# Performance work log

Measured on AMD Instinct MI355X. Metric: run time of the kernel, lower is better.

The kernel has to match this reference:

```python
import jax, jax.numpy as jnp
import numpy as np

B, L, D = 8, 2048, 64


def setup_inputs() -> dict:
    key = jax.random.key(0)
    kq, kk, kv = jax.random.split(key, 3)
    query = jax.random.normal(kq, (B, L, D), dtype=jnp.float32)
    key_t = jax.random.normal(kk, (B, L, D), dtype=jnp.float32)
    value = jax.random.normal(kv, (B, L, D), dtype=jnp.float32)
    return {"query": query, "key": key_t, "value": value}


def reference(query, key, value):
    d = query.shape[-1]
    # e = Q K^T / sqrt(d_k)   -> [B, Lq, Lk]
    scale = 1.0 / np.sqrt(float(d)).astype(np.float32)
    e = jnp.einsum("bqd,bkd->bqk", query, key) * scale
    # stable softmax over keys (matches exp(e - max)/sum in source)
    attention = jax.nn.softmax(e, axis=-1)
    # v = A V   -> [B, Lq, Dv]
    return jnp.einsum("bqk,bkd->bqd", attention, value)
```

## Files before the change

### kernel.cpp

```cpp
#include <hip/hip_runtime.h>


#define B_ 8
#define L_ 2048
#define D_ 64
#define NT 256

typedef _Float16 half8_t __attribute__((ext_vector_type(8)));
typedef _Float16 half4_t __attribute__((ext_vector_type(4)));
typedef float f32x4 __attribute__((ext_vector_type(4)));

#define SCALE_LOG2E 0.1803368801111244f

__global__ __launch_bounds__(NT) void prepass_frag(
    const float* __restrict__ K, const float* __restrict__ V,
    _Float16* __restrict__ K16F, _Float16* __restrict__ VT16F)
{
    const int blk = blockIdx.x;
    const int t = threadIdx.x;
    if (blk < 512) {
        const int b  = blk & 7;
        const int kt = blk >> 3;
        const int p    = t >> 6;
        const int lane = t & 63;
        const int quad = lane >> 4;
        const int l15  = lane & 15;
        const int s = p >> 1, c = p & 1;
        const int row = kt * 32 + s * 16 + l15;
        const float* kp = K + ((size_t)b * L_ + row) * D_ + c * 32 + quad * 8;
        const float4 f0 = *(const float4*)kp;
        const float4 f1 = *(const float4*)(kp + 4);
        half8_t w;
        w[0] = (_Float16)f0.x; w[1] = (_Float16)f0.y;
        w[2] = (_Float16)f0.z; w[3] = (_Float16)f0.w;
        w[4] = (_Float16)f1.x; w[5] = (_Float16)f1.y;
        w[6] = (_Float16)f1.z; w[7] = (_Float16)f1.w;
        *(half8_t*)&K16F[((size_t)(b * 64 + kt) * 4 + p) * 512 + lane * 8] = w;
    } else {
        const int vb = blk - 512;
        const int b  = vb & 7;
        const int kt = vb >> 3;
        #pragma unroll
        for (int i = 0; i < 2; ++i) {
            const int slot = i * NT + t;
            const int p    = slot >> 6;
            const int lane = slot & 63;
            const int quad = lane >> 4;
            const int l15  = lane & 15;
            const int d = p >> 1, ks = p & 1;
            const int row = kt * 32 + ks * 16 + quad * 4;
            const int col = d * 16 + l15;
            const float* vp = V + ((size_t)b * L_ + row) * D_ + col;
            half4_t a;
            a[0] = (_Float16)vp[0];
            a[1] = (_Float16)vp[D_];
            a[2] = (_Float16)vp[2 * D_];
            a[3] = (_Float16)vp[3 * D_];
            *(half4_t*)&VT16F[((size_t)(b * 64 + kt) * 4 + d) * 512 + lane * 8 + ks * 4] = a;
        }
    }
}


#define LOADK(KT, BK)                                                           \
    {                                                                           \
        const int ktc_ = (KT) & 63;                                             \
        _Pragma("unroll") for (int s = 0; s < 2; ++s)                           \
        _Pragma("unroll") for (int c = 0; c < 2; ++c)                           \
            BK[s][c] = *(const half8_t*)&KbF[((size_t)ktc_ * 4 + s * 2 + c) * 512 + lane * 8]; \
    }

#define LOADV(KT, AV)                                                           \
    {                                                                           \
        const int ktc_ = (KT) & 63;                                             \
        _Pragma("unroll") for (int d = 0; d < 4; ++d)                           \
            AV[d] = *(const half8_t*)&VbF[((size_t)ktc_ * 4 + d) * 512 + lane * 8]; \
    }

#define PROC(BK, AV)                                                            \
    {                                                                           \
        half4_t pb[2][2];                                                       \
        _Pragma("unroll") for (int ks = 0; ks < 2; ++ks)                        \
        _Pragma("unroll") for (int qs = 0; qs < 2; ++qs) {                      \
            f32x4 acc = (f32x4){0.f, 0.f, 0.f, 0.f};                            \
            acc = __builtin_amdgcn_mfma_f32_16x16x32_f16(BK[ks][0], bq[qs][0], acc, 0, 0, 0); \
            acc = __builtin_amdgcn_mfma_f32_16x16x32_f16(BK[ks][1], bq[qs][1], acc, 0, 0, 0); \
            const float p0 = __builtin_exp2f(acc[0]);                           \
            const float p1 = __builtin_exp2f(acc[1]);                           \
            const float p2 = __builtin_exp2f(acc[2]);                           \
            const float p3 = __builtin_exp2f(acc[3]);                           \
            lacc[qs] += (p0 + p1) + (p2 + p3);                                  \
            half4_t pv;                                                         \
            pv[0] = (_Float16)p0; pv[1] = (_Float16)p1;                         \
            pv[2] = (_Float16)p2; pv[3] = (_Float16)p3;                         \
            pb[ks][qs] = pv;                                                    \
        }                                                                       \
        _Pragma("unroll") for (int d = 0; d < 4; ++d) {                         \
            const half4_t alo = __builtin_shufflevector(AV[d], AV[d], 0, 1, 2, 3); \
            const half4_t ahi = __builtin_shufflevector(AV[d], AV[d], 4, 5, 6, 7); \
            _Pragma("unroll") for (int qs = 0; qs < 2; ++qs) {                  \
                ofr[qs][d] = __builtin_amdgcn_mfma_f32_16x16x16f16(alo, pb[0][qs], ofr[qs][d], 0, 0, 0); \
                ofr[qs][d] = __builtin_amdgcn_mfma_f32_16x16x16f16(ahi, pb[1][qs], ofr[qs][d], 0, 0, 0); \
            }                                                                   \
        }                                                                       \
    }

__global__ __launch_bounds__(1024) void attn_q64w16(
    const float* __restrict__ Q,
    const _Float16* __restrict__ K16F,
    const _Float16* __restrict__ VT16F,
    float* __restrict__ O)
{
    __shared__ float Ored[1024 * 17];
    __shared__ float Lred[512];

    const int t    = threadIdx.x;
    const int wave = t >> 6;
    const int lane = t & 63;
    const int quad = lane >> 4;
    const int l15  = lane & 15;
    const int kg   = wave >> 1;
    const int qg   = wave & 1;

    const int b   = blockIdx.x & 7;
    const int qbi = blockIdx.x >> 3;
    const int qb  = qbi * 64;
    const int q0  = qb + qg * 32;
    const int kt0 = kg * 8;

    const _Float16* KbF = K16F + (size_t)b * 64 * 4 * 512;
    const _Float16* VbF = VT16F + (size_t)b * 64 * 4 * 512;

    half8_t bq[2][2];
    #pragma unroll
    for (int qs = 0; qs < 2; ++qs) {
        const float* qp = Q + ((size_t)b * L_ + q0 + qs * 16 + l15) * D_ + quad * 8;
        #pragma unroll
        for (int c = 0; c < 2; ++c) {
            const float4 f0 = *(const float4*)(qp + c * 32);
            const float4 f1 = *(const float4*)(qp + c * 32 + 4);
            bq[qs][c][0] = (_Float16)(f0.x * SCALE_LOG2E);
            bq[qs][c][1] = (_Float16)(f0.y * SCALE_LOG2E);
            bq[qs][c][2] = (_Float16)(f0.z * SCALE_LOG2E);
            bq[qs][c][3] = (_Float16)(f0.w * SCALE_LOG2E);
            bq[qs][c][4] = (_Float16)(f1.x * SCALE_LOG2E);
            bq[qs][c][5] = (_Float16)(f1.y * SCALE_LOG2E);
            bq[qs][c][6] = (_Float16)(f1.z * SCALE_LOG2E);
            bq[qs][c][7] = (_Float16)(f1.w * SCALE_LOG2E);
        }
    }

    f32x4 ofr[2][4];
    #pragma unroll
    for (int qs = 0; qs < 2; ++qs)
        #pragma unroll
        for (int d = 0; d < 4; ++d)
            ofr[qs][d] = (f32x4){0.f, 0.f, 0.f, 0.f};
    float lacc[2] = {0.f, 0.f};

    half8_t bkA[2][2], bkB[2][2], av[4];
    LOADK(kt0, bkA);
    for (int it = 0; it < 4; ++it) {
        const int kta = kt0 + it * 2;
        LOADK(kta + 1, bkB);
        LOADV(kta, av);
        PROC(bkA, av);
        LOADK(kta + 2, bkA);
        LOADV(kta + 1, av);
        PROC(bkB, av);
    }

    float lsum[2];
    #pragma unroll
    for (int qs = 0; qs < 2; ++qs) {
        float v = lacc[qs];
        v += __shfl_xor(v, 16, 64);
        v += __shfl_xor(v, 32, 64);
        lsum[qs] = v;
    }
    if (quad == 0) {
        Lred[wave * 32 + l15]      = lsum[0];
        Lred[wave * 32 + 16 + l15] = lsum[1];
    }

    #pragma unroll
    for (int qs = 0; qs < 2; ++qs) {
        __syncthreads();
        float* dst = &Ored[(wave * 64 + lane) * 17];
        #pragma unroll
        for (int d = 0; d < 4; ++d)
            #pragma unroll
            for (int r = 0; r < 4; ++r)
                dst[d * 4 + r] = ofr[qs][d][r];
        __syncthreads();
        if (wave < 8) {
            const int rkg = wave >> 1;
            const int rqg = wave & 1;
            float lt = 0.f;
            #pragma unroll
            for (int k2 = 0; k2 < 8; ++k2)
                lt += Lred[(k2 * 2 + rqg) * 32 + qs * 16 + l15];
            const float inv = 1.0f / lt;
            f32x4 osum = (f32x4){0.f, 0.f, 0.f, 0.f};
            #pragma unroll
            for (int k2 = 0; k2 < 8; ++k2) {
                const float* src = &Ored[((k2 * 2 + rqg) * 64 + lane) * 17 + rkg * 4];
                osum[0] += src[0]; osum[1] += src[1];
                osum[2] += src[2]; osum[3] += src[3];
            }
            float4 outv;
            outv.x = osum[0] * inv; outv.y = osum[1] * inv;
            outv.z = osum[2] * inv; outv.w = osum[3] * inv;
            *(float4*)&O[((size_t)b * L_ + qb + rqg * 32 + qs * 16 + l15) * D_
                         + rkg * 16 + quad * 4] = outv;
        }
    }
}

#define KS 72
__global__ __launch_bounds__(NT) void attn_mfma_f16(
    const float* __restrict__ Q, const float* __restrict__ K,
    const float* __restrict__ V, float* __restrict__ O)
{
    __shared__ __align__(16) _Float16 Kt[64 * KS];
    __shared__ __align__(16) _Float16 Vt[D_ * KS];
    __shared__ __align__(16) _Float16 Pt[4][16 * KS];

    const int t = threadIdx.x;
    const int wave = t >> 6, lane = t & 63, quad = lane >> 4, l15 = lane & 15;
    const int bpb = L_ / 64;
    const int b = blockIdx.x / bpb;
    const int qb = (blockIdx.x % bpb) * 64 + wave * 16;
    const size_t boff = (size_t)b * L_ * D_;

    half8_t aq[2];
    {
        const float* qp = Q + boff + (size_t)(qb + l15) * D_ + quad * 8;
        #pragma unroll
        for (int c = 0; c < 2; ++c) {
            const float4* p4 = (const float4*)(qp + c * 32);
            const float4 f0 = p4[0], f1 = p4[1];
            aq[c][0] = (_Float16)f0.x; aq[c][1] = (_Float16)f0.y;
            aq[c][2] = (_Float16)f0.z; aq[c][3] = (_Float16)f0.w;
            aq[c][4] = (_Float16)f1.x; aq[c][5] = (_Float16)f1.y;
            aq[c][6] = (_Float16)f1.z; aq[c][7] = (_Float16)f1.w;
        }
    }
    f32x4 ofr[4];
    #pragma unroll
    for (int d = 0; d < 4; ++d) ofr[d] = (f32x4){0.f, 0.f, 0.f, 0.f};
    float lacc[4] = {0.f, 0.f, 0.f, 0.f};
    const int skey = t & 63, sdg = t >> 6;
    _Float16* Pw = &Pt[wave][0];

    for (int kt = 0; kt < L_ / 64; ++kt) {
        __syncthreads();
        {
            const float4* kg4 = (const float4*)(K + boff + (size_t)(kt * 64 + skey) * D_ + sdg * 16);
            const float4 f0 = kg4[0], f1 = kg4[1], f2 = kg4[2], f3 = kg4[3];
            half8_t w0, w1;
            w0[0] = (_Float16)f0.x; w0[1] = (_Float16)f0.y;
            w0[2] = (_Float16)f0.z; w0[3] = (_Float16)f0.w;
            w0[4] = (_Float16)f1.x; w0[5] = (_Float16)f1.y;
            w0[6] = (_Float16)f1.z; w0[7] = (_Float16)f1.w;
            w1[0] = (_Float16)f2.x; w1[1] = (_Float16)f2.y;
            w1[2] = (_Float16)f2.z; w1[3] = (_Float16)f2.w;
            w1[4] = (_Float16)f3.x; w1[5] = (_Float16)f3.y;
            w1[6] = (_Float16)f3.z; w1[7] = (_Float16)f3.w;
            *(half8_t*)&Kt[skey * KS + sdg * 16] = w0;
            *(half8_t*)&Kt[skey * KS + sdg * 16 + 8] = w1;
        }
        {
            const float4* vg4 = (const float4*)(V + boff + (size_t)(kt * 64 + skey) * D_ + sdg * 16);
            #pragma unroll
            for (int i = 0; i < 4; ++i) {
                const float4 f = vg4[i];
                const int d0 = sdg * 16 + i * 4;
                Vt[(d0 + 0) * KS + skey] = (_Float16)f.x;
                Vt[(d0 + 1) * KS + skey] = (_Float16)f.y;
                Vt[(d0 + 2) * KS + skey] = (_Float16)f.z;
                Vt[(d0 + 3) * KS + skey] = (_Float16)f.w;
            }
        }
        __syncthreads();
        #pragma unroll
        for (int s = 0; s < 4; ++s) {
            const half8_t bk0 = *(const half8_t*)&Kt[(s * 16 + l15) * KS + quad * 8];
            const half8_t bk1 = *(const half8_t*)&Kt[(s * 16 + l15) * KS + 32 + quad * 8];
            f32x4 sc = (f32x4){0.f, 0.f, 0.f, 0.f};
            sc = __builtin_amdgcn_mfma_f32_16x16x32_f16(aq[0], bk0, sc, 0, 0, 0);
            sc = __builtin_amdgcn_mfma_f32_16x16x32_f16(aq[1], bk1, sc, 0, 0, 0);
            #pragma unroll
            for (int r = 0; r < 4; ++r) {
                const float p = __expf(sc[r] * 0.125f);
                lacc[r] += p;
                Pw[(quad * 4 + r) * KS + s * 16 + l15] = (_Float16)p;
            }
        }
        __syncthreads();
        #pragma unroll
        for (int c = 0; c < 2; ++c) {
            const half8_t ap = *(const half8_t*)&Pw[l15 * KS + c * 32 + quad * 8];
            #pragma unroll
            for (int d = 0; d < 4; ++d) {
                const half8_t bv = *(const half8_t*)&Vt[(d * 16 + l15) * KS + c * 32 + quad * 8];
                ofr[d] = __builtin_amdgcn_mfma_f32_16x16x32_f16(ap, bv, ofr[d], 0, 0, 0);
            }
        }
    }
    #pragma unroll
    for (int r = 0; r < 4; ++r) {
        float v = lacc[r];
        v += __shfl_xor(v, 1, 64);
        v += __shfl_xor(v, 2, 64);
        v += __shfl_xor(v, 4, 64);
        v += __shfl_xor(v, 8, 64);
        lacc[r] = v;
    }
    #pragma unroll
    for (int r = 0; r < 4; ++r) {
        const float inv = 1.0f / lacc[r];
        float* orow = O + boff + (size_t)(qb + quad * 4 + r) * D_ + l15;
        #pragma unroll
        for (int d = 0; d < 4; ++d) orow[d * 16] = ofr[d][r] * inv;
    }
}

extern "C" void kernel_launch(void* const* d_in, const int* in_sizes, int n_in,
                              void* d_out, int out_size, void* d_ws, size_t ws_size,
                              hipStream_t stream) {
    const float* Q = (const float*)d_in[0];
    const float* K = (const float*)d_in[1];
    const float* V = (const float*)d_in[2];
    float* O = (float*)d_out;

    if (ws_size >= (size_t)8 * 1024 * 1024) {
        _Float16* K16F  = (_Float16*)d_ws;
        _Float16* VT16F = K16F + (size_t)1048576;
        prepass_frag<<<1024, NT, 0, stream>>>(K, V, K16F, VT16F);
        attn_q64w16<<<256, 1024, 0, stream>>>(Q, K16F, VT16F, O);
    } else {
        attn_mfma_f16<<<256, NT, 0, stream>>>(Q, K, V, O);
    }
}
```

Before: 83.98 us.

## Stage K/V fragments through double-buffered shared memory instead of direct global loads

```diff
diff --git a/kernel.cpp b/kernel.cpp
--- a/kernel.cpp
+++ b/kernel.cpp
@@ -62,29 +62,20 @@
 }
 
 
-#define LOADK(KT, BK)                                                           \
+#define PROCL(CB)                                                               \
     {                                                                           \
-        const int ktc_ = (KT) & 63;                                             \
+        const _Float16* Kt = &FR[(CB) + kg * 4096];                             \
+        const _Float16* Vt = Kt + 2048;                                         \
+        half8_t bk[2][2];                                                       \
         _Pragma("unroll") for (int s = 0; s < 2; ++s)                           \
         _Pragma("unroll") for (int c = 0; c < 2; ++c)                           \
-            BK[s][c] = *(const half8_t*)&KbF[((size_t)ktc_ * 4 + s * 2 + c) * 512 + lane * 8]; \
-    }
-
-#define LOADV(KT, AV)                                                           \
-    {                                                                           \
-        const int ktc_ = (KT) & 63;                                             \
-        _Pragma("unroll") for (int d = 0; d < 4; ++d)                           \
-            AV[d] = *(const half8_t*)&VbF[((size_t)ktc_ * 4 + d) * 512 + lane * 8]; \
-    }
-
-#define PROC(BK, AV)                                                            \
-    {                                                                           \
+            bk[s][c] = *(const half8_t*)&Kt[(s * 2 + c) * 512 + lane * 8];      \
         half4_t pb[2][2];                                                       \
         _Pragma("unroll") for (int ks = 0; ks < 2; ++ks)                        \
         _Pragma("unroll") for (int qs = 0; qs < 2; ++qs) {                      \
             f32x4 acc = (f32x4){0.f, 0.f, 0.f, 0.f};                            \
-            acc = __builtin_amdgcn_mfma_f32_16x16x32_f16(BK[ks][0], bq[qs][0], acc, 0, 0, 0); \
-            acc = __builtin_amdgcn_mfma_f32_16x16x32_f16(BK[ks][1], bq[qs][1], acc, 0, 0, 0); \
+            acc = __builtin_amdgcn_mfma_f32_16x16x32_f16(bk[ks][0], bq[qs][0], acc, 0, 0, 0); \
+            acc = __builtin_amdgcn_mfma_f32_16x16x32_f16(bk[ks][1], bq[qs][1], acc, 0, 0, 0); \
             const float p0 = __builtin_exp2f(acc[0]);                           \
             const float p1 = __builtin_exp2f(acc[1]);                           \
             const float p2 = __builtin_exp2f(acc[2]);                           \
@@ -96,8 +87,9 @@
             pb[ks][qs] = pv;                                                    \
         }                                                                       \
         _Pragma("unroll") for (int d = 0; d < 4; ++d) {                         \
-            const half4_t alo = __builtin_shufflevector(AV[d], AV[d], 0, 1, 2, 3); \
-            const half4_t ahi = __builtin_shufflevector(AV[d], AV[d], 4, 5, 6, 7); \
+            const half8_t av8 = *(const half8_t*)&Vt[d * 512 + lane * 8];       \
+            const half4_t alo = __builtin_shufflevector(av8, av8, 0, 1, 2, 3);  \
+            const half4_t ahi = __builtin_shufflevector(av8, av8, 4, 5, 6, 7);  \
             _Pragma("unroll") for (int qs = 0; qs < 2; ++qs) {                  \
                 ofr[qs][d] = __builtin_amdgcn_mfma_f32_16x16x16f16(alo, pb[0][qs], ofr[qs][d], 0, 0, 0); \
                 ofr[qs][d] = __builtin_amdgcn_mfma_f32_16x16x16f16(ahi, pb[1][qs], ofr[qs][d], 0, 0, 0); \
@@ -105,14 +97,21 @@
         }                                                                       \
     }
 
-__global__ __launch_bounds__(1024) void attn_q64w16(
+#define SGLOAD(TT)                                                              \
+    _Pragma("unroll") for (int j = 0; j < 4; ++j)                               \
+        kf[j] = *(const float4*)(sb[j] + (size_t)(TT) * 2048);
+
+#define SSWRITE(BUF)                                                            \
+    _Pragma("unroll") for (int j = 0; j < 4; ++j)                               \
+        *(float4*)&FR[(BUF) * 32768 + sdst[j]] = kf[j];
+
+__global__ __launch_bounds__(1024) void attn_shared(
     const float* __restrict__ Q,
     const _Float16* __restrict__ K16F,
     const _Float16* __restrict__ VT16F,
     float* __restrict__ O)
 {
-    __shared__ float Ored[1024 * 17];
-    __shared__ float Lred[512];
+    __shared__ __align__(16) _Float16 FR[65536];
 
     const int t    = threadIdx.x;
     const int wave = t >> 6;
@@ -126,10 +125,21 @@
     const int qbi = blockIdx.x >> 3;
     const int qb  = qbi * 64;
     const int q0  = qb + qg * 32;
-    const int kt0 = kg * 8;
 
     const _Float16* KbF = K16F + (size_t)b * 64 * 4 * 512;
     const _Float16* VbF = VT16F + (size_t)b * 64 * 4 * 512;
+
+    const _Float16* sb[4];
+    int sdst[4];
+    #pragma unroll
+    for (int j = 0; j < 4; ++j) {
+        const int s = j * 1024 + t;
+        const int skg  = s >> 9;
+        const int half = (s >> 8) & 1;
+        const int o16  = s & 255;
+        sb[j] = (half ? VbF : KbF) + (size_t)skg * 16384 + o16 * 8;
+        sdst[j] = s * 8;
+    }
 
     half8_t bq[2][2];
     #pragma unroll
@@ -158,16 +168,20 @@
             ofr[qs][d] = (f32x4){0.f, 0.f, 0.f, 0.f};
     float lacc[2] = {0.f, 0.f};
 
-    half8_t bkA[2][2], bkB[2][2], av[4];
-    LOADK(kt0, bkA);
-    for (int it = 0; it < 4; ++it) {
-        const int kta = kt0 + it * 2;
-        LOADK(kta + 1, bkB);
-        LOADV(kta, av);
-        PROC(bkA, av);
-        LOADK(kta + 2, bkA);
-        LOADV(kta + 1, av);
-        PROC(bkB, av);
+    float4 kf[4];
+    SGLOAD(0);
+    SSWRITE(0);
+    SGLOAD(1);
+    __syncthreads();
+
+    for (int tt = 0; tt < 8; ++tt) {
+        const int cb = (tt & 1) * 32768;
+        if (tt < 7) {
+            SSWRITE((tt & 1) ^ 1);
+            if (tt < 6) SGLOAD(tt + 2);
+        }
+        PROCL(cb);
+        __syncthreads();
     }
 
     float lsum[2];
@@ -178,6 +192,8 @@
         v += __shfl_xor(v, 32, 64);
         lsum[qs] = v;
     }
+    float* Ored = (float*)&FR[0];
+    float* Lred = Ored + 17408;
     if (quad == 0) {
         Lred[wave * 32 + l15]      = lsum[0];
         Lred[wave * 32 + 16 + l15] = lsum[1];
@@ -338,7 +354,7 @@
         _Float16* K16F  = (_Float16*)d_ws;
         _Float16* VT16F = K16F + (size_t)1048576;
         prepass_frag<<<1024, NT, 0, stream>>>(K, V, K16F, VT16F);
-        attn_q64w16<<<256, 1024, 0, stream>>>(Q, K16F, VT16F, O);
+        attn_shared<<<256, 1024, 0, stream>>>(Q, K16F, VT16F, O);
     } else {
         attn_mfma_f16<<<256, NT, 0, stream>>>(Q, K, V, O);
     }
```

Result: slower. 111.8 us (+33.1%).
